# Kernel optimization log

Measured on AMD Instinct MI355X. Metric: run time of the kernel, lower is better.

Reference implementation:

```python
import jax, jax.numpy as jnp
import numpy as np

N, E, G = 50000, 800000, 64          # nodes, edges, graphs in batch
F, HG, HL = 64, 128, 128             # node feat, graph hidden, lin hidden
AVG_LOG = float(np.log(9.0))         # from deg histogram [0]*8+[1]: log(8+1)


def setup_inputs() -> dict:
    key = jax.random.key(0)
    ks = jax.random.split(key, 24)
    def w(k, shape):
        return 0.1 * jax.random.normal(k, shape, jnp.float32)
    return {
        "x": jax.random.normal(ks[0], (N, F), jnp.float32),
        "edge_index": jax.random.randint(ks[1], (2, E), 0, N),
        "edge_attr": jax.random.normal(ks[2], (E, 1), jnp.float32),
        "batch": jnp.sort(jax.random.randint(ks[3], (N,), 0, G)),
        # PNAConv params (towers=1, pre_layers=1, post_layers=1, edge_dim=1)
        "W_edge": w(ks[4], (1, F)),      "b_edge": w(ks[5], (F,)),
        "W_pre": w(ks[6], (3 * F, F)),   "b_pre": w(ks[7], (F,)),
        "W_post": w(ks[8], (13 * F, HG)), "b_post": w(ks[9], (HG,)),
        "W_lin": w(ks[10], (HG, HG)),    "b_lin": w(ks[11], (HG,)),
        # bn1 / fc2 / bn2
        "g1": jnp.ones((HG,)), "be1": jnp.zeros((HG,)),
        "W2": w(ks[12], (HG, HL)), "b2": w(ks[13], (HL,)),
        "g2": jnp.ones((HL,)), "be2": jnp.zeros((HL,)),
        # one resnet block: fc/bn/fc/bn
        "Wr1": w(ks[14], (HL, HL)), "br1": w(ks[15], (HL,)),
        "gr1": jnp.ones((HL,)), "ber1": jnp.zeros((HL,)),
        "Wr2": w(ks[16], (HL, HL)), "br2": w(ks[17], (HL,)),
        "gr2": jnp.ones((HL,)), "ber2": jnp.zeros((HL,)),
        "W_out": w(ks[18], (HL, 1)), "b_out": w(ks[19], (1,)),
    }


def _bn(z, g, b):
    # BatchNorm1d, training mode: biased batch stats, eps=1e-5
    mu = z.mean(0)
    var = ((z - mu) ** 2).mean(0)
    return (z - mu) * jax.lax.rsqrt(var + 1e-5) * g + b


def _pna(x, edge_index, edge_attr, W_edge, b_edge, W_pre, b_pre,
         W_post, b_post, W_lin, b_lin):
    src, dst = edge_index[0], edge_index[1]  # messages flow j->i, aggregate at dst
    e = edge_attr @ W_edge + b_edge                               # [E, F]
    m = jnp.concatenate([x[dst], x[src], e], -1) @ W_pre + b_pre  # [E, F]
    ones_e = jnp.ones((m.shape[0],), m.dtype)
    cnt = jax.ops.segment_sum(ones_e, dst, N)                     # in-degree
    cnt1 = jnp.maximum(cnt, 1.0)
    mean = jax.ops.segment_sum(m, dst, N) / cnt1[:, None]
    mean2 = jax.ops.segment_sum(m * m, dst, N) / cnt1[:, None]
    std = jnp.sqrt(jax.nn.relu(mean2 - mean * mean) + 1e-5)
    has = (cnt > 0)[:, None]
    mn = jnp.where(has, jax.ops.segment_min(m, dst, N), 0.0)
    mx = jnp.where(has, jax.ops.segment_max(m, dst, N), 0.0)
    agg = jnp.concatenate([mean, mn, mx, std], -1)                # [N, 4F]
    amp = (jnp.log(cnt1 + 1.0) / AVG_LOG)[:, None]                # amplification scaler
    out = jnp.concatenate([agg, agg * amp, agg / amp], -1)        # [N, 12F]
    out = jnp.concatenate([x, out], -1) @ W_post + b_post         # [N, HG]
    return out @ W_lin + b_lin                                    # [N, HG]


def reference(x, edge_index, edge_attr, batch,
              W_edge, b_edge, W_pre, b_pre, W_post, b_post, W_lin, b_lin,
              g1, be1, W2, b2, g2, be2,
              Wr1, br1, gr1, ber1, Wr2, br2, gr2, ber2,
              W_out, b_out):
    h = _pna(x, edge_index, edge_attr, W_edge, b_edge, W_pre, b_pre,
             W_post, b_post, W_lin, b_lin)
    # global_mean_pool over graphs
    gc = jnp.maximum(jax.ops.segment_sum(jnp.ones((h.shape[0],), h.dtype), batch, G), 1.0)
    z = jax.ops.segment_sum(h, batch, G) / gc[:, None]            # [G, HG]
    z = jax.nn.relu(_bn(z, g1, be1))
    z = jax.nn.relu(_bn(z @ W2 + b2, g2, be2))
    r = z
    z = jax.nn.relu(_bn(z @ Wr1 + br1, gr1, ber1))
    z = jax.nn.relu(_bn(z @ Wr2 + br2, gr2, ber2) + r)
    return z @ W_out + b_out                                      # [G, 1]
```

## Files before the change

### kernel.cpp

```cpp
#include <hip/hip_runtime.h>
#include <hip/hip_bf16.h>

using bf16 = __hip_bfloat16;

#define F 64
#define HG 128
#define HL 128
#define AVG_LOG_INV 0.45511961331341866f
#define BSH 5
#define BNODES 32
#define BCAP 1024
#define BTILE 8192
#define NBMAX 1664

typedef short short8 __attribute__((ext_vector_type(8)));
typedef float floatx4 __attribute__((ext_vector_type(4)));

__device__ __forceinline__ float b2f(bf16 v) { return __bfloat162float(v); }
__device__ __forceinline__ bf16 f2b(float v) { return __float2bfloat16(v); }
__device__ __forceinline__ short f2bs(float v) { bf16 h = f2b(v); return *(short*)&h; }

__device__ __forceinline__ unsigned packbf2(float x, float y) {
    bf16 a = f2b(x), b = f2b(y);
    unsigned short ua = *(unsigned short*)&a, ub = *(unsigned short*)&b;
    return ((unsigned)ub << 16) | (unsigned)ua;
}

__device__ __forceinline__ float wave_sum(float v) {
    #pragma unroll
    for (int m = 32; m > 0; m >>= 1) v += __shfl_xor(v, m);
    return v;
}

__global__ void k_init(int* __restrict__ gcur, float* __restrict__ gfeat,
                       int* __restrict__ gcnt, int NB, int GF, int G,
                       const float* __restrict__ W_edge, const float* __restrict__ b_edge,
                       const float* __restrict__ W_pre, const float* __restrict__ b_pre,
                       float* __restrict__ uc) {
    if (blockIdx.x == gridDim.x - 1) {
        int f = threadIdx.x;
        if (f < 64) {
            float u = 0.f, c = b_pre[f];
            for (int k = 0; k < 64; k++) {
                float w3 = W_pre[(128 + k) * 64 + f];
                u += W_edge[k] * w3;
                c += b_edge[k] * w3;
            }
            uc[f] = u; uc[64 + f] = c;
        } else if (f - 64 < G) {
            gcnt[f - 64] = 0;
        }
        return;
    }
    int i = blockIdx.x * 256 + threadIdx.x;
    if (i < NB) gcur[i] = 0;
    if (i < GF) gfeat[i] = 0.f;
}

__global__ void k_ab_mfma(const float* __restrict__ x, const float* __restrict__ W_pre,
                          bf16* __restrict__ AB, int N) {
    __shared__ unsigned short wt[128 * 72];
    for (int idx = threadIdx.x; idx < 8192; idx += 256) {
        int k = idx >> 7, m = idx & 127;
        float v = W_pre[((m & 64) + k) * 64 + (m & 63)];
        wt[m * 72 + k] = (unsigned short)f2bs(v);
    }
    __syncthreads();

    int lane = threadIdx.x & 63;
    int row = lane & 15, quad = lane >> 4;
    int w = (blockIdx.x * blockDim.x + threadIdx.x) >> 6;
    int nwaves = (gridDim.x * blockDim.x) >> 6;
    int ntiles = (N + 15) >> 4;

    for (int tile = w; tile < ntiles; tile += nwaves) {
        int m0 = tile << 4;
        int node_a = m0 + row; if (node_a >= N) node_a = N - 1;
        short8 a[2];
        #pragma unroll
        for (int h = 0; h < 2; h++) {
            const float* xp = x + (size_t)node_a * 64 + h * 32 + quad * 8;
            floatx4 v0 = *(const floatx4*)xp;
            floatx4 v1 = *(const floatx4*)(xp + 4);
            #pragma unroll
            for (int j = 0; j < 4; j++) { a[h][j] = f2bs(v0[j]); a[h][4 + j] = f2bs(v1[j]); }
        }
        #pragma unroll
        for (int t = 0; t < 8; t++) {
            int fbase = t * 16;
            floatx4 c = {0.f, 0.f, 0.f, 0.f};
            #pragma unroll
            for (int h = 0; h < 2; h++) {
                short8 b = *(const short8*)(wt + (fbase + row) * 72 + h * 32 + quad * 8);
                c = __builtin_amdgcn_mfma_f32_16x16x32_bf16(a[h], b, c, 0, 0, 0);
            }
            #pragma unroll
            for (int r = 0; r < 4; r++) {
                int node = m0 + quad * 4 + r;
                if (node < N) AB[(size_t)node * 128 + fbase + row] = f2b(c[r]);
            }
        }
    }
}

__global__ void k_bucket(const int* __restrict__ ei, const float* __restrict__ ea,
                         int* __restrict__ gcur, int2* __restrict__ gout,
                         int E, int NB) {
    __shared__ int2 recs[BTILE];
    __shared__ int hist[NBMAX], gst[NBMAX], lrk[NBMAX];
    int t = threadIdx.x;
    for (int b = t; b < NB; b += 1024) hist[b] = 0;
    __syncthreads();
    int base = blockIdx.x * BTILE;
    int lim = E - base; if (lim > BTILE) lim = BTILE;
    for (int i = t; i < lim; i += 1024) {
        int e = base + i;
        int src = ei[e], dst = ei[E + e];
        recs[i] = make_int2((dst << 16) | src, __float_as_int(ea[e]));
        atomicAdd(&hist[dst >> BSH], 1);
    }
    __syncthreads();
    for (int b = t; b < NB; b += 1024) {
        int h = hist[b];
        lrk[b] = 0;
        gst[b] = (h > 0) ? atomicAdd(&gcur[b], h) : 0;
    }
    __syncthreads();
    for (int i = t; i < lim; i += 1024) {
        int2 r = recs[i];
        int b = ((unsigned)r.x) >> (16 + BSH);
        int k = atomicAdd(&lrk[b], 1);
        int pos = gst[b] + k;
        if (pos < BCAP) gout[(size_t)b * BCAP + pos] = r;
    }
}

__global__ void k_edge(const bf16* __restrict__ AB, const int2* __restrict__ gout,
                       const int* __restrict__ gcur, const float* __restrict__ uc,
                       bf16* __restrict__ agg, float* __restrict__ ampv, int N) {
    __shared__ int2 recs[BCAP], sortd[BCAP];
    __shared__ int ncnt[BNODES], nofs[BNODES], nrank[BNODES];
    int t = threadIdx.x;
    int b = blockIdx.x;
    int nn = N - b * BNODES; if (nn > BNODES) nn = BNODES;
    int ecnt = gcur[b]; if (ecnt > BCAP) ecnt = BCAP;

    for (int i = t; i < ecnt; i += 512) recs[i] = gout[(size_t)b * BCAP + i];
    if (t < BNODES) { ncnt[t] = 0; nrank[t] = 0; }
    __syncthreads();
    for (int i = t; i < ecnt; i += 512)
        atomicAdd(&ncnt[((unsigned)recs[i].x >> 16) & (BNODES - 1)], 1);
    __syncthreads();
    if (t < BNODES) {
        int v = ncnt[t], inc = v;
        #pragma unroll
        for (int m = 1; m < BNODES; m <<= 1) { int u = __shfl_up(inc, m); if (t >= m) inc += u; }
        nofs[t] = inc - v;
    }
    __syncthreads();
    for (int i = t; i < ecnt; i += 512) {
        int2 r = recs[i];
        int nl = ((unsigned)r.x >> 16) & (BNODES - 1);
        int k = atomicAdd(&nrank[nl], 1);
        sortd[nofs[nl] + k] = r;
    }
    __syncthreads();

    int lane = t & 63, w = t >> 6;
    int half = lane & 31, hi32 = lane >> 5;
    float2 u2 = *(const float2*)(uc + 2 * half);
    float2 c2 = *(const float2*)(uc + 64 + 2 * half);

    for (int nl = w; nl < nn; nl += 8) {
        int n = b * BNODES + nl;
        int lo = nofs[nl], cnt = ncnt[nl], hi = lo + cnt;

        unsigned apack = *(const unsigned*)(AB + (size_t)n * 128 + 2 * half);
        float acx = __uint_as_float(apack << 16) + c2.x;
        float acy = __uint_as_float(apack & 0xffff0000u) + c2.y;

        float sx = 0.f, sy = 0.f, qx = 0.f, qy = 0.f;
        float mnx = 3.4e38f, mny = 3.4e38f, mxx = -3.4e38f, mxy = -3.4e38f;

        auto acc2 = [&](unsigned bp, float eav) {
            float bx = __uint_as_float(bp << 16);
            float by = __uint_as_float(bp & 0xffff0000u);
            float m0 = fmaf(eav, u2.x, acx) + bx;
            float m1 = fmaf(eav, u2.y, acy) + by;
            sx += m0; qx = fmaf(m0, m0, qx);
            sy += m1; qy = fmaf(m1, m1, qy);
            mnx = fminf(mnx, m0); mxx = fmaxf(mxx, m0);
            mny = fminf(mny, m1); mxy = fmaxf(mxy, m1);
        };
        auto gaddr = [&](int sn) {
            return (const unsigned*)(AB + (size_t)sn * 128 + 64 + 2 * half);
        };

        for (int base = lo; base < hi; base += 64) {
            int nb = hi - base; if (nb > 64) nb = 64;
            int2 rec = (lane < nb) ? sortd[base + lane] : make_int2(0, 0);
            int vsn = rec.x & 0xFFFF;
            float vea = __int_as_float(rec.y);
            int i = 0;
            for (; i + 8 <= nb; i += 8) {
                int sn0 = __shfl(vsn, i + hi32);
                int sn1 = __shfl(vsn, i + 2 + hi32);
                int sn2 = __shfl(vsn, i + 4 + hi32);
                int sn3 = __shfl(vsn, i + 6 + hi32);
                float e0 = __shfl(vea, i + hi32);
                float e1 = __shfl(vea, i + 2 + hi32);
                float e2 = __shfl(vea, i + 4 + hi32);
                float e3 = __shfl(vea, i + 6 + hi32);
                unsigned b0 = *gaddr(sn0);
                unsigned b1 = *gaddr(sn1);
                unsigned b2 = *gaddr(sn2);
                unsigned b3 = *gaddr(sn3);
                acc2(b0, e0); acc2(b1, e1); acc2(b2, e2); acc2(b3, e3);
            }
            for (; i + 2 <= nb; i += 2) {
                int   sn = __shfl(vsn, i + hi32);
                float ev = __shfl(vea, i + hi32);
                acc2(*gaddr(sn), ev);
            }
            if (i < nb) {
                int   sn = __shfl(vsn, i);
                float ev = __shfl(vea, i);
                unsigned bp = *gaddr(sn);
                if (hi32 == 0) acc2(bp, ev);
            }
        }
        sx += __shfl_xor(sx, 32); sy += __shfl_xor(sy, 32);
        qx += __shfl_xor(qx, 32); qy += __shfl_xor(qy, 32);
        mnx = fminf(mnx, __shfl_xor(mnx, 32)); mny = fminf(mny, __shfl_xor(mny, 32));
        mxx = fmaxf(mxx, __shfl_xor(mxx, 32)); mxy = fmaxf(mxy, __shfl_xor(mxy, 32));

        float c1 = (cnt > 0) ? (float)cnt : 1.f;
        float inv = 1.f / c1;
        float mex = sx * inv, mey = sy * inv;
        float vx = qx * inv - mex * mex; if (vx < 0.f) vx = 0.f;
        float vy = qy * inv - mey * mey; if (vy < 0.f) vy = 0.f;
        float sdx = sqrtf(vx + 1e-5f), sdy = sqrtf(vy + 1e-5f);
        if (cnt == 0) { mnx = mny = mxx = mxy = 0.f; }

        size_t ob = (size_t)n * 256 + 2 * half;
        if (hi32 == 0) {
            *(unsigned*)(agg + ob)       = packbf2(mex, mey);
            *(unsigned*)(agg + ob + 64)  = packbf2(mnx, mny);
        } else {
            *(unsigned*)(agg + ob + 128) = packbf2(mxx, mxy);
            *(unsigned*)(agg + ob + 192) = packbf2(sdx, sdy);
        }
        if (lane == 0) ampv[n] = logf(c1 + 1.f) * AVG_LOG_INV;
    }
}

__global__ void k_greduce2(const float* __restrict__ x, const bf16* __restrict__ agg,
                           const float* __restrict__ ampv, const int* __restrict__ batch,
                           float* __restrict__ gfeat, int* __restrict__ gcnt,
                           int N, int chunk) {
    int t = threadIdx.x;
    int lo = blockIdx.x * chunk;
    int hi = lo + chunk; if (hi > N) hi = N;
    if (lo >= hi) return;
    int curg = batch[lo];
    float s1 = 0.f, s2 = 0.f, s3 = 0.f, sx = 0.f;
    int cnt = 0;
    for (int n = lo; n < hi; n++) {
        int g = batch[n];
        if (g != curg) {
            float* gf = gfeat + (size_t)curg * 832;
            atomicAdd(&gf[64 + t], s1);
            atomicAdd(&gf[320 + t], s2);
            atomicAdd(&gf[576 + t], s3);
            if (t < 64) atomicAdd(&gf[t], sx);
            if (t == 0) atomicAdd(&gcnt[curg], cnt);
            s1 = s2 = s3 = sx = 0.f; cnt = 0; curg = g;
        }
        float amp = ampv[n];
        float av = b2f(agg[(size_t)n * 256 + t]);
        s1 += av; s2 += av * amp; s3 += av / amp;
        if (t < 64) sx += x[(size_t)n * 64 + t];
        cnt++;
    }
    float* gf = gfeat + (size_t)curg * 832;
    atomicAdd(&gf[64 + t], s1);
    atomicAdd(&gf[320 + t], s2);
    atomicAdd(&gf[576 + t], s3);
    if (t < 64) atomicAdd(&gf[t], sx);
    if (t == 0) atomicAdd(&gcnt[curg], cnt);
}

__global__ void k_post1(const float* __restrict__ gfeat, const int* __restrict__ gcnt,
                        const float* __restrict__ W_post, const float* __restrict__ b_post,
                        const float* __restrict__ W_lin, const float* __restrict__ b_lin,
                        float* __restrict__ Zin) {
    int g = blockIdx.x, j = threadIdx.x;
    __shared__ float feat[832];
    __shared__ float z1[128];
    int cg = gcnt[g];
    float r = 1.f / ((cg > 0) ? (float)cg : 1.f);
    for (int i = j; i < 832; i += 128) feat[i] = gfeat[(size_t)g * 832 + i] * r;
    __syncthreads();
    float acc = b_post[j];
    for (int k = 0; k < 832; k++) acc += feat[k] * W_post[k * 128 + j];
    z1[j] = acc;
    __syncthreads();
    float a2 = b_lin[j];
    for (int k = 0; k < 128; k++) a2 += z1[k] * W_lin[k * 128 + j];
    if (cg == 0) a2 = 0.f;
    Zin[g * 128 + j] = a2;
}

__global__ void k_mlpcol(const float* __restrict__ in, const float* __restrict__ W,
                         const float* __restrict__ bias,
                         const float* __restrict__ gamma, const float* __restrict__ beta,
                         const float* __restrict__ res,
                         const float* __restrict__ g_in, const float* __restrict__ be_in,
                         float* __restrict__ outp) {
    __shared__ float A[64 * 129];
    __shared__ float part[4 * 64];
    int t = threadIdx.x;
    int j = blockIdx.x;

    for (int i = t; i < 8192; i += 256) A[(i >> 7) * 129 + (i & 127)] = in[i];
    __syncthreads();

    if (g_in) {
        if (t < 128) {
            int c = t;
            float mu = 0.f;
            for (int r = 0; r < 64; r++) mu += A[r * 129 + c];
            mu *= (1.f / 64.f);
            float var = 0.f;
            for (int r = 0; r < 64; r++) { float d = A[r * 129 + c] - mu; var += d * d; }
            var *= (1.f / 64.f);
            float sc = rsqrtf(var + 1e-5f) * g_in[c], sh = be_in[c];
            for (int r = 0; r < 64; r++) {
                float v = (A[r * 129 + c] - mu) * sc + sh;
                A[r * 129 + c] = v > 0.f ? v : 0.f;
            }
        }
        __syncthreads();
    }

    int r = t & 63, q = t >> 6;
    float acc = 0.f;
    int k0 = q * 32;
    #pragma unroll
    for (int k = 0; k < 32; k++) acc += A[r * 129 + k0 + k] * W[(k0 + k) * 128 + j];
    part[q * 64 + r] = acc;
    __syncthreads();

    if (t < 64) {
        float v = part[t] + part[64 + t] + part[128 + t] + part[192 + t] + bias[j];
        float mu = wave_sum(v) * (1.f / 64.f);
        float d = v - mu;
        float var = wave_sum(d * d) * (1.f / 64.f);
        float o = d * rsqrtf(var + 1e-5f) * gamma[j] + beta[j];
        if (res) o += res[t * 128 + j];
        outp[t * 128 + j] = o > 0.f ? o : 0.f;
    }
}

__global__ void k_out(const float* __restrict__ z4, const float* __restrict__ W_out,
                      const float* b_out, float* __restrict__ out) {
    int g = threadIdx.x;
    float acc = b_out[0];
    for (int j = 0; j < 128; j++) acc += z4[g * 128 + j] * W_out[j];
    out[g] = acc;
}

extern "C" void kernel_launch(void* const* d_in, const int* in_sizes, int n_in,
                              void* d_out, int out_size, void* d_ws, size_t ws_size,
                              hipStream_t stream) {
    const float* x      = (const float*)d_in[0];
    const int*   ei     = (const int*)d_in[1];
    const float* ea     = (const float*)d_in[2];
    const int*   batch  = (const int*)d_in[3];
    const float* W_edge = (const float*)d_in[4];
    const float* b_edge = (const float*)d_in[5];
    const float* W_pre  = (const float*)d_in[6];
    const float* b_pre  = (const float*)d_in[7];
    const float* W_post = (const float*)d_in[8];
    const float* b_post = (const float*)d_in[9];
    const float* W_lin  = (const float*)d_in[10];
    const float* b_lin  = (const float*)d_in[11];
    const float* g1     = (const float*)d_in[12];
    const float* be1    = (const float*)d_in[13];
    const float* W2     = (const float*)d_in[14];
    const float* b2     = (const float*)d_in[15];
    const float* g2     = (const float*)d_in[16];
    const float* be2    = (const float*)d_in[17];
    const float* Wr1    = (const float*)d_in[18];
    const float* br1    = (const float*)d_in[19];
    const float* gr1    = (const float*)d_in[20];
    const float* ber1   = (const float*)d_in[21];
    const float* Wr2    = (const float*)d_in[22];
    const float* br2    = (const float*)d_in[23];
    const float* gr2    = (const float*)d_in[24];
    const float* ber2   = (const float*)d_in[25];
    const float* W_out  = (const float*)d_in[26];
    const float* b_out  = (const float*)d_in[27];
    float* out = (float*)d_out;

    const int N = in_sizes[0] / F;
    const int E = in_sizes[1] / 2;
    const int G = out_size;
    const int NB = (N + BNODES - 1) >> BSH;

    char* p = (char*)d_ws;
    auto alloc = [&](size_t nbytes) { void* r = p; p += (nbytes + 255) & ~(size_t)255; return r; };
    bf16*  AB     = (bf16*)alloc((size_t)N * 128 * sizeof(bf16));
    bf16*  agg    = (bf16*)alloc((size_t)N * 256 * sizeof(bf16));
    float* ampv   = (float*)alloc((size_t)N * sizeof(float));
    int*   gcur   = (int*)alloc((size_t)NB * sizeof(int));
    int2*  gout   = (int2*)alloc((size_t)NB * BCAP * sizeof(int2));
    float* uc     = (float*)alloc(128 * sizeof(float));
    float* gfeat  = (float*)alloc((size_t)G * 832 * sizeof(float));
    int*   gcnt   = (int*)alloc((size_t)G * sizeof(int));
    float* Zin    = (float*)alloc(64 * 128 * sizeof(float));
    float* z2b    = (float*)alloc(64 * 128 * sizeof(float));
    float* z3b    = (float*)alloc(64 * 128 * sizeof(float));
    float* z4b    = (float*)alloc(64 * 128 * sizeof(float));

    const int GF = G * 832;
    int initb = (GF + 255) / 256;
    if ((NB + 255) / 256 > initb) initb = (NB + 255) / 256;
    const int GRB = 1024;
    const int GRCH = (N + GRB - 1) / GRB;
    const int ABB = ((N + 15) / 16 + 3) / 4;
    const int NBT = (E + BTILE - 1) / BTILE;

    k_init<<<initb + 1, 256, 0, stream>>>(gcur, gfeat, gcnt, NB, GF, G,
                                          W_edge, b_edge, W_pre, b_pre, uc);
    k_ab_mfma<<<ABB, 256, 0, stream>>>(x, W_pre, AB, N);
    k_bucket<<<NBT, 1024, 0, stream>>>(ei, ea, gcur, gout, E, NB);
    k_edge<<<NB, 512, 0, stream>>>(AB, gout, gcur, uc, agg, ampv, N);
    k_greduce2<<<GRB, 256, 0, stream>>>(x, agg, ampv, batch, gfeat, gcnt, N, GRCH);
    k_post1<<<G, 128, 0, stream>>>(gfeat, gcnt, W_post, b_post, W_lin, b_lin, Zin);
    k_mlpcol<<<HG, 256, 0, stream>>>(Zin, W2, b2, g2, be2, nullptr, g1, be1, z2b);
    k_mlpcol<<<HL, 256, 0, stream>>>(z2b, Wr1, br1, gr1, ber1, nullptr, nullptr, nullptr, z3b);
    k_mlpcol<<<HL, 256, 0, stream>>>(z3b, Wr2, br2, gr2, ber2, z2b, nullptr, nullptr, z4b);
    k_out<<<1, 64, 0, stream>>>(z4b, W_out, b_out, out);
}
```

Measured before the change: 240.3 us.

## Fuse graph mean-pool reduction into edge kernel and merge init into AB kernel

The per-node aggregates are no longer written to a bf16 agg buffer and re-read by a separate reduction kernel. The edge kernel now accumulates the graph-level sums directly into shared-memory partials for the block's first and last graph, then flushes them with global atomics. The init kernel is folded into the AB MFMA kernel, and the bucket kernel loads edges with 128-bit vector loads. This removes two launches and the N×256 intermediate round trip, at the cost of many shared atomics per node. It also assumes a 32-node block spans at most two graphs, falling back to global atomics otherwise. The zeroing of gcur/gfeat now happens in k_ab_mfma on the same stream before k_bucket, which keeps the ordering correct.

```diff
diff --git a/kernel.cpp b/kernel.cpp
--- a/kernel.cpp
+++ b/kernel.cpp
@@ -20,45 +20,34 @@
 __device__ __forceinline__ bf16 f2b(float v) { return __float2bfloat16(v); }
 __device__ __forceinline__ short f2bs(float v) { bf16 h = f2b(v); return *(short*)&h; }
 
-__device__ __forceinline__ unsigned packbf2(float x, float y) {
-    bf16 a = f2b(x), b = f2b(y);
-    unsigned short ua = *(unsigned short*)&a, ub = *(unsigned short*)&b;
-    return ((unsigned)ub << 16) | (unsigned)ua;
-}
-
 __device__ __forceinline__ float wave_sum(float v) {
     #pragma unroll
     for (int m = 32; m > 0; m >>= 1) v += __shfl_xor(v, m);
     return v;
 }
 
-__global__ void k_init(int* __restrict__ gcur, float* __restrict__ gfeat,
-                       int* __restrict__ gcnt, int NB, int GF, int G,
-                       const float* __restrict__ W_edge, const float* __restrict__ b_edge,
-                       const float* __restrict__ W_pre, const float* __restrict__ b_pre,
-                       float* __restrict__ uc) {
-    if (blockIdx.x == gridDim.x - 1) {
+__global__ void k_ab_mfma(const float* __restrict__ x, const float* __restrict__ W_pre,
+                          bf16* __restrict__ AB, int N,
+                          int* __restrict__ gcur, float* __restrict__ gfeat,
+                          int* __restrict__ gcnt, int NB, int GF, int G,
+                          const float* __restrict__ W_edge, const float* __restrict__ b_edge,
+                          const float* __restrict__ b_pre, float* __restrict__ uc) {
+    int gtid = blockIdx.x * blockDim.x + threadIdx.x;
+    int gstr = gridDim.x * blockDim.x;
+    for (int i = gtid; i < GF; i += gstr) gfeat[i] = 0.f;
+    for (int i = gtid; i < NB; i += gstr) gcur[i] = 0;
+    for (int i = gtid; i < G; i += gstr) gcnt[i] = 0;
+    if (blockIdx.x == 0 && threadIdx.x < 64) {
         int f = threadIdx.x;
-        if (f < 64) {
-            float u = 0.f, c = b_pre[f];
-            for (int k = 0; k < 64; k++) {
-                float w3 = W_pre[(128 + k) * 64 + f];
-                u += W_edge[k] * w3;
-                c += b_edge[k] * w3;
-            }
-            uc[f] = u; uc[64 + f] = c;
-        } else if (f - 64 < G) {
-            gcnt[f - 64] = 0;
-        }
-        return;
-    }
-    int i = blockIdx.x * 256 + threadIdx.x;
-    if (i < NB) gcur[i] = 0;
-    if (i < GF) gfeat[i] = 0.f;
-}
-
-__global__ void k_ab_mfma(const float* __restrict__ x, const float* __restrict__ W_pre,
-                          bf16* __restrict__ AB, int N) {
+        float u = 0.f, c = b_pre[f];
+        for (int k = 0; k < 64; k++) {
+            float w3 = W_pre[(128 + k) * 64 + f];
+            u += W_edge[k] * w3;
+            c += b_edge[k] * w3;
+        }
+        uc[f] = u; uc[64 + f] = c;
+    }
+
     __shared__ unsigned short wt[128 * 72];
     for (int idx = threadIdx.x; idx < 8192; idx += 256) {
         int k = idx >> 7, m = idx & 127;
@@ -113,7 +102,24 @@
     __syncthreads();
     int base = blockIdx.x * BTILE;
     int lim = E - base; if (lim > BTILE) lim = BTILE;
-    for (int i = t; i < lim; i += 1024) {
+    int nq = lim >> 2;
+    const int4* src4 = (const int4*)(ei + base);
+    const int4* dst4 = (const int4*)(ei + E + base);
+    const float4* ea4 = (const float4*)(ea + base);
+    for (int q = t; q < nq; q += 1024) {
+        int4 s = src4[q], d = dst4[q];
+        float4 v = ea4[q];
+        int i = q * 4;
+        recs[i]     = make_int2((d.x << 16) | s.x, __float_as_int(v.x));
+        recs[i + 1] = make_int2((d.y << 16) | s.y, __float_as_int(v.y));
+        recs[i + 2] = make_int2((d.z << 16) | s.z, __float_as_int(v.z));
+        recs[i + 3] = make_int2((d.w << 16) | s.w, __float_as_int(v.w));
+        atomicAdd(&hist[d.x >> BSH], 1);
+        atomicAdd(&hist[d.y >> BSH], 1);
+        atomicAdd(&hist[d.z >> BSH], 1);
+        atomicAdd(&hist[d.w >> BSH], 1);
+    }
+    for (int i = (nq << 2) + t; i < lim; i += 1024) {
         int e = base + i;
         int src = ei[e], dst = ei[E + e];
         recs[i] = make_int2((dst << 16) | src, __float_as_int(ea[e]));
@@ -137,14 +143,21 @@
 
 __global__ void k_edge(const bf16* __restrict__ AB, const int2* __restrict__ gout,
                        const int* __restrict__ gcur, const float* __restrict__ uc,
-                       bf16* __restrict__ agg, float* __restrict__ ampv, int N) {
+                       const float* __restrict__ x, const int* __restrict__ batch,
+                       float* __restrict__ gfeat, int* __restrict__ gcnt, int N) {
     __shared__ int2 recs[BCAP], sortd[BCAP];
-    __shared__ int ncnt[BNODES], nofs[BNODES], nrank[BNODES];
+    __shared__ int ncnt[BNODES], nofs[BNODES], nrank[BNODES], gbatch[BNODES];
+    __shared__ float gpart[2 * 832];
+    __shared__ int lcnt[2];
     int t = threadIdx.x;
     int b = blockIdx.x;
-    int nn = N - b * BNODES; if (nn > BNODES) nn = BNODES;
+    int n0 = b * BNODES;
+    int nn = N - n0; if (nn > BNODES) nn = BNODES;
     int ecnt = gcur[b]; if (ecnt > BCAP) ecnt = BCAP;
 
+    for (int i = t; i < 1664; i += 512) gpart[i] = 0.f;
+    if (t < 2) lcnt[t] = 0;
+    if (t < nn) gbatch[t] = batch[n0 + t];
     for (int i = t; i < ecnt; i += 512) recs[i] = gout[(size_t)b * BCAP + i];
     if (t < BNODES) { ncnt[t] = 0; nrank[t] = 0; }
     __syncthreads();
@@ -170,9 +183,11 @@
     int half = lane & 31, hi32 = lane >> 5;
     float2 u2 = *(const float2*)(uc + 2 * half);
     float2 c2 = *(const float2*)(uc + 64 + 2 * half);
+    int g0 = gbatch[0];
+    int g1v = gbatch[nn - 1];
 
     for (int nl = w; nl < nn; nl += 8) {
-        int n = b * BNODES + nl;
+        int n = n0 + nl;
         int lo = nofs[nl], cnt = ncnt[nl], hi = lo + cnt;
 
         unsigned apack = *(const unsigned*)(AB + (size_t)n * 128 + 2 * half);
@@ -242,52 +257,45 @@
         float sdx = sqrtf(vx + 1e-5f), sdy = sqrtf(vy + 1e-5f);
         if (cnt == 0) { mnx = mny = mxx = mxy = 0.f; }
 
-        size_t ob = (size_t)n * 256 + 2 * half;
-        if (hi32 == 0) {
-            *(unsigned*)(agg + ob)       = packbf2(mex, mey);
-            *(unsigned*)(agg + ob + 64)  = packbf2(mnx, mny);
+        float amp = logf(c1 + 1.f) * AVG_LOG_INV;
+        float ra = 1.f / amp;
+        float a0 = hi32 ? mxx : mex, a1 = hi32 ? mxy : mey;
+        float b0v = hi32 ? sdx : mnx, b1v = hi32 ? sdy : mny;
+        int o0 = (hi32 ? 192 : 64) + 2 * half;
+        int o1 = (hi32 ? 256 : 128) + 2 * half;
+        float xv = x[(size_t)n * 64 + lane];
+        int gg = gbatch[nl];
+        int idx = (gg == g0) ? 0 : ((gg == g1v) ? 1 : -1);
+        if (idx >= 0) {
+            float* gp = gpart + idx * 832;
+            atomicAdd(&gp[lane], xv);
+            atomicAdd(&gp[o0], a0);        atomicAdd(&gp[o0 + 1], a1);
+            atomicAdd(&gp[o0 + 256], a0 * amp); atomicAdd(&gp[o0 + 257], a1 * amp);
+            atomicAdd(&gp[o0 + 512], a0 * ra);  atomicAdd(&gp[o0 + 513], a1 * ra);
+            atomicAdd(&gp[o1], b0v);       atomicAdd(&gp[o1 + 1], b1v);
+            atomicAdd(&gp[o1 + 256], b0v * amp); atomicAdd(&gp[o1 + 257], b1v * amp);
+            atomicAdd(&gp[o1 + 512], b0v * ra);  atomicAdd(&gp[o1 + 513], b1v * ra);
+            if (lane == 0) atomicAdd(&lcnt[idx], 1);
         } else {
-            *(unsigned*)(agg + ob + 128) = packbf2(mxx, mxy);
-            *(unsigned*)(agg + ob + 192) = packbf2(sdx, sdy);
-        }
-        if (lane == 0) ampv[n] = logf(c1 + 1.f) * AVG_LOG_INV;
-    }
-}
-
-__global__ void k_greduce2(const float* __restrict__ x, const bf16* __restrict__ agg,
-                           const float* __restrict__ ampv, const int* __restrict__ batch,
-                           float* __restrict__ gfeat, int* __restrict__ gcnt,
-                           int N, int chunk) {
-    int t = threadIdx.x;
-    int lo = blockIdx.x * chunk;
-    int hi = lo + chunk; if (hi > N) hi = N;
-    if (lo >= hi) return;
-    int curg = batch[lo];
-    float s1 = 0.f, s2 = 0.f, s3 = 0.f, sx = 0.f;
-    int cnt = 0;
-    for (int n = lo; n < hi; n++) {
-        int g = batch[n];
-        if (g != curg) {
-            float* gf = gfeat + (size_t)curg * 832;
-            atomicAdd(&gf[64 + t], s1);
-            atomicAdd(&gf[320 + t], s2);
-            atomicAdd(&gf[576 + t], s3);
-            if (t < 64) atomicAdd(&gf[t], sx);
-            if (t == 0) atomicAdd(&gcnt[curg], cnt);
-            s1 = s2 = s3 = sx = 0.f; cnt = 0; curg = g;
-        }
-        float amp = ampv[n];
-        float av = b2f(agg[(size_t)n * 256 + t]);
-        s1 += av; s2 += av * amp; s3 += av / amp;
-        if (t < 64) sx += x[(size_t)n * 64 + t];
-        cnt++;
-    }
-    float* gf = gfeat + (size_t)curg * 832;
-    atomicAdd(&gf[64 + t], s1);
-    atomicAdd(&gf[320 + t], s2);
-    atomicAdd(&gf[576 + t], s3);
-    if (t < 64) atomicAdd(&gf[t], sx);
-    if (t == 0) atomicAdd(&gcnt[curg], cnt);
+            float* gp = gfeat + (size_t)gg * 832;
+            atomicAdd(&gp[lane], xv);
+            atomicAdd(&gp[o0], a0);        atomicAdd(&gp[o0 + 1], a1);
+            atomicAdd(&gp[o0 + 256], a0 * amp); atomicAdd(&gp[o0 + 257], a1 * amp);
+            atomicAdd(&gp[o0 + 512], a0 * ra);  atomicAdd(&gp[o0 + 513], a1 * ra);
+            atomicAdd(&gp[o1], b0v);       atomicAdd(&gp[o1 + 1], b1v);
+            atomicAdd(&gp[o1 + 256], b0v * amp); atomicAdd(&gp[o1 + 257], b1v * amp);
+            atomicAdd(&gp[o1 + 512], b0v * ra);  atomicAdd(&gp[o1 + 513], b1v * ra);
+            if (lane == 0) atomicAdd(&gcnt[gg], 1);
+        }
+    }
+    __syncthreads();
+    for (int i = t; i < 832; i += 512) atomicAdd(&gfeat[(size_t)g0 * 832 + i], gpart[i]);
+    if (g1v > g0)
+        for (int i = t; i < 832; i += 512) atomicAdd(&gfeat[(size_t)g1v * 832 + i], gpart[832 + i]);
+    if (t == 0) {
+        atomicAdd(&gcnt[g0], lcnt[0]);
+        if (g1v > g0) atomicAdd(&gcnt[g1v], lcnt[1]);
+    }
 }
 
 __global__ void k_post1(const float* __restrict__ gfeat, const int* __restrict__ gcnt,
@@ -411,8 +419,6 @@
     char* p = (char*)d_ws;
     auto alloc = [&](size_t nbytes) { void* r = p; p += (nbytes + 255) & ~(size_t)255; return r; };
     bf16*  AB     = (bf16*)alloc((size_t)N * 128 * sizeof(bf16));
-    bf16*  agg    = (bf16*)alloc((size_t)N * 256 * sizeof(bf16));
-    float* ampv   = (float*)alloc((size_t)N * sizeof(float));
     int*   gcur   = (int*)alloc((size_t)NB * sizeof(int));
     int2*  gout   = (int2*)alloc((size_t)NB * BCAP * sizeof(int2));
     float* uc     = (float*)alloc(128 * sizeof(float));
@@ -424,19 +430,13 @@
     float* z4b    = (float*)alloc(64 * 128 * sizeof(float));
 
     const int GF = G * 832;
-    int initb = (GF + 255) / 256;
-    if ((NB + 255) / 256 > initb) initb = (NB + 255) / 256;
-    const int GRB = 1024;
-    const int GRCH = (N + GRB - 1) / GRB;
     const int ABB = ((N + 15) / 16 + 3) / 4;
     const int NBT = (E + BTILE - 1) / BTILE;
 
-    k_init<<<initb + 1, 256, 0, stream>>>(gcur, gfeat, gcnt, NB, GF, G,
-                                          W_edge, b_edge, W_pre, b_pre, uc);
-    k_ab_mfma<<<ABB, 256, 0, stream>>>(x, W_pre, AB, N);
+    k_ab_mfma<<<ABB, 256, 0, stream>>>(x, W_pre, AB, N, gcur, gfeat, gcnt, NB, GF, G,
+                                       W_edge, b_edge, b_pre, uc);
     k_bucket<<<NBT, 1024, 0, stream>>>(ei, ea, gcur, gout, E, NB);
-    k_edge<<<NB, 512, 0, stream>>>(AB, gout, gcur, uc, agg, ampv, N);
-    k_greduce2<<<GRB, 256, 0, stream>>>(x, agg, ampv, batch, gfeat, gcnt, N, GRCH);
+    k_edge<<<NB, 512, 0, stream>>>(AB, gout, gcur, uc, x, batch, gfeat, gcnt, N);
     k_post1<<<G, 128, 0, stream>>>(gfeat, gcnt, W_post, b_post, W_lin, b_lin, Zin);
     k_mlpcol<<<HG, 256, 0, stream>>>(Zin, W2, b2, g2, be2, nullptr, g1, be1, z2b);
     k_mlpcol<<<HL, 256, 0, stream>>>(z2b, Wr1, br1, gr1, ber1, nullptr, nullptr, nullptr, z3b);
```

New measurement: 436.3 us. +81.5%, slower.
